# Kernel optimization log

Measured on AMD Instinct MI355X. Metric: run time of the kernel, lower is better.

The kernel has to match this reference:

```python
import jax, jax.numpy as jnp
import numpy as np

TOP_K = 8          # n_activated_experts
ROUTE_SCALE = 2.5  # route_scale


def setup_inputs() -> dict:
    key = jax.random.key(0)
    k1, k2, k3 = jax.random.split(key, 3)
    T, D, E = 16384, 7168, 256
    x = jax.random.normal(k1, (T, D), dtype=jnp.float32)
    # nn.Linear weight layout: [out_features, in_features]
    W = jax.random.normal(k2, (E, D), dtype=jnp.float32) * (1.0 / np.sqrt(D))
    bias = jax.random.normal(k3, (E,), dtype=jnp.float32) * 0.01
    return {"x": x, "W": W, "bias": bias}


def reference(x, W, bias):
    # logits: [T, E] = x [T, D] @ W.T [D, E]
    logits = jnp.einsum("td,ed->te", x, W)
    scores = jax.nn.sigmoid(logits)              # original_scores
    biased = scores + bias                       # bias only affects expert selection
    _, indices = jax.lax.top_k(biased, TOP_K)    # [T, K] int32
    weights = jnp.take_along_axis(scores, indices, axis=-1)  # gather unbiased scores
    weights = weights / jnp.sum(weights, axis=-1, keepdims=True)  # sigmoid renorm
    weights = weights * ROUTE_SCALE
    return weights.astype(x.dtype), indices
```

## Files before the change

### kernel.cpp

```cpp
#include <hip/hip_runtime.h>
#include <cmath>

namespace {

typedef _Float16 half8 __attribute__((ext_vector_type(8)));
typedef float f32x4 __attribute__((ext_vector_type(4)));

constexpr int kTokens = 16384;
constexpr int kD      = 7168;
constexpr int kE      = 256;
constexpr int kTopK   = 8;
constexpr float kRouteScale = 2.5f;

constexpr int BM     = 32;
constexpr int BK     = 32;
constexpr int KSTEP  = 128;
constexpr int NT     = kD / BK;
constexpr int NSTEP  = kD / KSTEP;
constexpr float kS  = 4096.0f;
constexpr float kC  = 0.000244140625f;
constexpr size_t kWsTileB = 32768;
constexpr size_t kWsNeed  = (size_t)NT * kWsTileB;

__device__ inline void convoy_barrier() {
    asm volatile("s_waitcnt lgkmcnt(0)" ::: "memory");
    __builtin_amdgcn_s_barrier();
    asm volatile("" ::: "memory");
}

__global__ void wconv_kernel(const float* __restrict__ W, unsigned char* __restrict__ ws)
{
    const int e = blockIdx.x;
    const int t = threadIdx.x;
    const float* src = W + (size_t)e * kD + (size_t)t * 8;
    float v[8];
    *reinterpret_cast<float4*>(v)     = *reinterpret_cast<const float4*>(src);
    *reinterpret_cast<float4*>(v + 4) = *reinterpret_cast<const float4*>(src + 4);
    half8 h, l;
#pragma unroll
    for (int j = 0; j < 8; ++j) {
        _Float16 hh = (_Float16)v[j];
        h[j] = hh;
        l[j] = (_Float16)((v[j] - (float)hh) * kS);
    }
    const int kt = t >> 2;
    const int kg = t & 3;
    const size_t off = (size_t)kt * kWsTileB +
                       (size_t)(((e >> 4) << 6) + (kg << 4) + (e & 15)) * 16;
    *reinterpret_cast<half8*>(ws + off)         = h;
    *reinterpret_cast<half8*>(ws + off + 16384) = l;
}

__global__ __launch_bounds__(512, 4)
void gate_mfma(const float* __restrict__ x,
               const unsigned char* __restrict__ wst,
               const float* __restrict__ bias,
               float* __restrict__ out)
{
    __shared__ unsigned char lds[32896];

    const int t    = threadIdx.x;
    const int lane = t & 63;
    const int wid  = t >> 6;
    const int kk0  = wid & 3;
    const int m0   = blockIdx.x * BM;
    const int l15  = lane & 15;
    const int lg   = lane >> 4;

    const int srow = t >> 4;
    const int skc  = t & 15;
    const unsigned waddr = (unsigned)(((skc >> 2) << 12) + ((srow >> 4) << 10) +
                                      ((skc & 3) << 8) + ((((srow & 15) ^ skc) & 15) << 4));
    const float* xsrc = x + (size_t)(m0 + srow) * kD + (size_t)(skc * 8);

    const unsigned char* wb = wst + (size_t)(wid * 2) * 1024 + (size_t)lane * 16;

    f32x4 acc0[2][2], acc1[2][2], accL[2][2];
#pragma unroll
    for (int i = 0; i < 2; ++i)
#pragma unroll
        for (int j = 0; j < 2; ++j) {
            acc0[i][j] = f32x4{0.f,0.f,0.f,0.f};
            acc1[i][j] = f32x4{0.f,0.f,0.f,0.f};
            accL[i][j] = f32x4{0.f,0.f,0.f,0.f};
        }

    half8 bh[2][2];
    half8 bl[2][2];
    half8 axh[2][2];
    half8 axm[2][2];

    auto LOADB = [&](int pp, int kt) {
        const unsigned char* p = wb + (size_t)kt * kWsTileB;
        bh[pp][0] = *reinterpret_cast<const half8*>(p);
        bh[pp][1] = *reinterpret_cast<const half8*>(p + 1024);
        bl[pp][0] = *reinterpret_cast<const half8*>(p + 16384);
        bl[pp][1] = *reinterpret_cast<const half8*>(p + 16384 + 1024);
    };
    auto LDA = [&](int pp, unsigned bufc, int kk) {
        const unsigned base = bufc + (unsigned)(kk << 12) + (unsigned)(lg << 8) +
                              (unsigned)((((l15 ^ ((kk << 2) + lg)) & 15) << 4));
        axh[pp][0] = *reinterpret_cast<const half8*>(&lds[base]);
        axh[pp][1] = *reinterpret_cast<const half8*>(&lds[base + 1024]);
        axm[pp][0] = *reinterpret_cast<const half8*>(&lds[base + 2048]);
        axm[pp][1] = *reinterpret_cast<const half8*>(&lds[base + 3072]);
    };
    auto WRITESTEP = [&](unsigned base, const float4& a, const float4& b) {
        float v[8];
        *reinterpret_cast<float4*>(v)     = a;
        *reinterpret_cast<float4*>(v + 4) = b;
        half8 h0, h1;
#pragma unroll
        for (int j = 0; j < 8; ++j) {
            const _Float16 hh = (_Float16)v[j];
            h0[j] = hh;
            h1[j] = (_Float16)((v[j] - (float)hh) * kS);
        }
        *reinterpret_cast<half8*>(&lds[base + waddr])        = h0;
        *reinterpret_cast<half8*>(&lds[base + waddr + 2048]) = h1;
    };

    {
        float4 a = *reinterpret_cast<const float4*>(xsrc);
        float4 b = *reinterpret_cast<const float4*>(xsrc + 4);
        LOADB(0, kk0);
        WRITESTEP(0, a, b);
    }
    convoy_barrier();

    for (int s = 0; s < NSTEP; ++s) {
        const unsigned bufc = (unsigned)((s & 1) << 14);
        const unsigned bufn = (unsigned)(((s + 1) & 1) << 14);
        const bool pre = (s + 1 < NSTEP);

        LDA(0, bufc, kk0);
        float4 nv0{0,0,0,0}, nv1{0,0,0,0};
        if (pre) {
            const float* p = xsrc + (s + 1) * KSTEP;
            nv0 = *reinterpret_cast<const float4*>(p);
            nv1 = *reinterpret_cast<const float4*>(p + 4);
        }

#pragma unroll
        for (int n = 0; n < 4; ++n) {
            const int kk = (kk0 + n) & 3;
            const int pp = n & 1;
            const int kt_next = (n < 3) ? (s * 4 + ((kk0 + n + 1) & 3))
                                        : ((s + 1) * 4 + kk0);
            if (kt_next < NT) LOADB(pp ^ 1, kt_next);
            if (n < 3)        LDA(pp ^ 1, bufc, (kk0 + n + 1) & 3);
#pragma unroll
            for (int i = 0; i < 2; ++i)
#pragma unroll
                for (int j = 0; j < 2; ++j)
                    acc0[i][j] = __builtin_amdgcn_mfma_f32_16x16x32_f16(axh[pp][i], bh[pp][j], acc0[i][j], 0, 0, 0);
#pragma unroll
            for (int i = 0; i < 2; ++i)
#pragma unroll
                for (int j = 0; j < 2; ++j)
                    acc1[i][j] = __builtin_amdgcn_mfma_f32_16x16x32_f16(axm[pp][i], bh[pp][j], acc1[i][j], 0, 0, 0);
#pragma unroll
            for (int i = 0; i < 2; ++i)
#pragma unroll
                for (int j = 0; j < 2; ++j)
                    acc1[i][j] = __builtin_amdgcn_mfma_f32_16x16x32_f16(axh[pp][i], bl[pp][j], acc1[i][j], 0, 0, 0);
        }

        if (pre) WRITESTEP(bufn, nv0, nv1);

        if (((s + 1) & 7) == 0) {
#pragma unroll
            for (int i = 0; i < 2; ++i)
#pragma unroll
                for (int j = 0; j < 2; ++j) {
                    accL[i][j] += acc0[i][j];
                    acc0[i][j] = f32x4{0.f,0.f,0.f,0.f};
                }
        }
        convoy_barrier();
    }

    float (*sc)[257] = reinterpret_cast<float (*)[257]>(lds);
#pragma unroll
    for (int j = 0; j < 2; ++j) {
        const int col  = wid * 32 + j * 16 + l15;
        const float bv = bias[col];
#pragma unroll
        for (int i = 0; i < 2; ++i) {
            f32x4 z = (accL[i][j] + acc0[i][j]) + kC * acc1[i][j];
#pragma unroll
            for (int r = 0; r < 4; ++r) {
                const int row = i * 16 + lg * 4 + r;
                const float s = 1.0f / (1.0f + expf(-z[r]));
                sc[row][col] = s + bv;
            }
        }
    }
    __syncthreads();

    const int rr = t >> 4;
    const int g  = t & 15;

    float cval[kTopK];
    int   cidx[kTopK];

#pragma unroll
    for (int r = 0; r < kTopK; ++r) {
        float best = -INFINITY;
        int   bi   = kE;
        const float* rowp = sc[rr] + g * 16;
#pragma unroll 8
        for (int c = 0; c < 16; ++c) {
            const float v  = rowp[c];
            const int   ci = g * 16 + c;
            if (v > best || (v == best && ci < bi)) { best = v; bi = ci; }
        }
#pragma unroll
        for (int off = 8; off > 0; off >>= 1) {
            const float ov = __shfl_xor(best, off, 16);
            const int   oi = __shfl_xor(bi,   off, 16);
            if (ov > best || (ov == best && oi < bi)) { best = ov; bi = oi; }
        }
        cval[r] = best;
        cidx[r] = bi;
        if ((bi >> 4) == g) sc[rr][bi] = -INFINITY;
    }

    if (g == 0) {
        float uw[kTopK];
        float wsum = 0.0f;
#pragma unroll
        for (int r = 0; r < kTopK; ++r) {
            uw[r] = cval[r] - bias[cidx[r]];
            wsum += uw[r];
        }
        const float scale = kRouteScale / wsum;
        const size_t grow = (size_t)(m0 + rr);
#pragma unroll
        for (int r = 0; r < kTopK; ++r)
            out[grow * kTopK + r] = uw[r] * scale;
#pragma unroll
        for (int r = 0; r < kTopK; ++r)
            out[(size_t)kTokens * kTopK + grow * kTopK + r] = (float)cidx[r];
    }
}

constexpr int FBM = 32;
constexpr int FBK = 32;
constexpr int XS_STRIDE = 36;
constexpr int SC_STRIDE = 260;

__global__ __launch_bounds__(256, 2)
void gate_fused(const float* __restrict__ x,
                const float* __restrict__ W,
                const float* __restrict__ bias,
                float* __restrict__ out)
{
    __shared__ float smem[FBK * XS_STRIDE + FBK * kE];
    float (*xs)[XS_STRIDE] = reinterpret_cast<float (*)[XS_STRIDE]>(smem);
    float (*ws)[kE]        = reinterpret_cast<float (*)[kE]>(smem + FBK * XS_STRIDE);
    float (*sc)[SC_STRIDE] = reinterpret_cast<float (*)[SC_STRIDE]>(smem);

    const int t  = threadIdx.x;
    const int tx = t & 31;
    const int ty = t >> 5;
    const int m0 = blockIdx.x * FBM;
    const int lm = t >> 3;
    const int lc = t & 7;

    float acc[4][8];
    float cmp[4][8];
#pragma unroll
    for (int i = 0; i < 4; ++i)
#pragma unroll
        for (int j = 0; j < 8; ++j) { acc[i][j] = 0.0f; cmp[i][j] = 0.0f; }

    const float* xrow = x + (size_t)(m0 + lm) * kD;
    const float* wrow = W + (size_t)t * kD;

    for (int k0 = 0; k0 < kD; k0 += FBK) {
        float4 xv = *reinterpret_cast<const float4*>(xrow + k0 + 4 * lc);
        float4 wv[8];
#pragma unroll
        for (int i = 0; i < 8; ++i)
            wv[i] = *reinterpret_cast<const float4*>(wrow + k0 + 4 * i);
        __syncthreads();
        xs[4 * lc + 0][lm] = xv.x; xs[4 * lc + 1][lm] = xv.y;
        xs[4 * lc + 2][lm] = xv.z; xs[4 * lc + 3][lm] = xv.w;
#pragma unroll
        for (int i = 0; i < 8; ++i) {
            ws[4 * i + 0][t] = wv[i].x; ws[4 * i + 1][t] = wv[i].y;
            ws[4 * i + 2][t] = wv[i].z; ws[4 * i + 3][t] = wv[i].w;
        }
        __syncthreads();
        float p[4][8];
#pragma unroll
        for (int i = 0; i < 4; ++i)
#pragma unroll
            for (int j = 0; j < 8; ++j) p[i][j] = 0.0f;
#pragma unroll
        for (int k = 0; k < FBK; ++k) {
            float a[4], b[8];
            *reinterpret_cast<float4*>(a)     = *reinterpret_cast<const float4*>(&xs[k][4 * ty]);
            *reinterpret_cast<float4*>(b)     = *reinterpret_cast<const float4*>(&ws[k][4 * tx]);
            *reinterpret_cast<float4*>(b + 4) = *reinterpret_cast<const float4*>(&ws[k][128 + 4 * tx]);
#pragma unroll
            for (int i = 0; i < 4; ++i)
#pragma unroll
                for (int j = 0; j < 8; ++j)
                    p[i][j] = fmaf(a[i], b[j], p[i][j]);
        }
#pragma unroll
        for (int i = 0; i < 4; ++i)
#pragma unroll
            for (int j = 0; j < 8; ++j) {
                const float y = p[i][j] - cmp[i][j];
                const float s = acc[i][j] + y;
                cmp[i][j] = (s - acc[i][j]) - y;
                acc[i][j] = s;
            }
    }
    __syncthreads();
#pragma unroll
    for (int i = 0; i < 4; ++i) {
        const int row = 4 * ty + i;
#pragma unroll
        for (int j = 0; j < 8; ++j) {
            const int col = (j < 4) ? (4 * tx + j) : (128 + 4 * tx + (j - 4));
            const float s = 1.0f / (1.0f + expf(-acc[i][j]));
            sc[row][col] = s + bias[col];
        }
    }
    __syncthreads();
    const int rr = t >> 3;
    const int g  = t & 7;
    float cval[kTopK];
    int   cidx[kTopK];
#pragma unroll
    for (int r = 0; r < kTopK; ++r) {
        float best = -INFINITY;
        int   bi   = kE;
        const float* rowp = sc[rr] + g * 32;
#pragma unroll 8
        for (int c = 0; c < 32; ++c) {
            const float v  = rowp[c];
            const int   ci = g * 32 + c;
            if (v > best || (v == best && ci < bi)) { best = v; bi = ci; }
        }
#pragma unroll
        for (int off = 4; off > 0; off >>= 1) {
            const float ov = __shfl_xor(best, off, 8);
            const int   oi = __shfl_xor(bi,   off, 8);
            if (ov > best || (ov == best && oi < bi)) { best = ov; bi = oi; }
        }
        cval[r] = best; cidx[r] = bi;
        if ((bi >> 5) == g) sc[rr][bi] = -INFINITY;
        __syncthreads();
    }
    if (g == 0) {
        float uw[kTopK];
        float wsum = 0.0f;
#pragma unroll
        for (int r = 0; r < kTopK; ++r) { uw[r] = cval[r] - bias[cidx[r]]; wsum += uw[r]; }
        const float scale = kRouteScale / wsum;
        const size_t grow = (size_t)(m0 + rr);
#pragma unroll
        for (int r = 0; r < kTopK; ++r) out[grow * kTopK + r] = uw[r] * scale;
#pragma unroll
        for (int r = 0; r < kTopK; ++r)
            out[(size_t)kTokens * kTopK + grow * kTopK + r] = (float)cidx[r];
    }
}

}

extern "C" void kernel_launch(void* const* d_in, const int* in_sizes, int n_in,
                              void* d_out, int out_size, void* d_ws, size_t ws_size,
                              hipStream_t stream)
{
    const float* x    = (const float*)d_in[0];
    const float* W    = (const float*)d_in[1];
    const float* bias = (const float*)d_in[2];
    float* out = (float*)d_out;

    if (ws_size >= kWsNeed) {
        unsigned char* ws = (unsigned char*)d_ws;
        hipLaunchKernelGGL(wconv_kernel, dim3(kE), dim3(kD / 8), 0, stream, W, ws);
        hipLaunchKernelGGL(gate_mfma, dim3(kTokens / BM), dim3(512), 0, stream, x, ws, bias, out);
    } else {
        hipLaunchKernelGGL(gate_fused, dim3(kTokens / FBM), dim3(256), 0, stream, x, W, bias, out);
    }
}
```

Before: 278.6 us.

## Double per-block token tile to 64 rows and halve the K step

```diff
diff --git a/kernel.cpp b/kernel.cpp
--- a/kernel.cpp
+++ b/kernel.cpp
@@ -12,9 +12,9 @@
 constexpr int kTopK   = 8;
 constexpr float kRouteScale = 2.5f;
 
-constexpr int BM     = 32;
+constexpr int BM     = 64;
 constexpr int BK     = 32;
-constexpr int KSTEP  = 128;
+constexpr int KSTEP  = 64;
 constexpr int NT     = kD / BK;
 constexpr int NSTEP  = kD / KSTEP;
 constexpr float kS  = 4096.0f;
@@ -51,33 +51,32 @@
     *reinterpret_cast<half8*>(ws + off + 16384) = l;
 }
 
-__global__ __launch_bounds__(512, 4)
+__global__ __launch_bounds__(512, 2)
 void gate_mfma(const float* __restrict__ x,
                const unsigned char* __restrict__ wst,
                const float* __restrict__ bias,
                float* __restrict__ out)
 {
-    __shared__ unsigned char lds[32896];
+    __shared__ unsigned char lds[65792];
 
     const int t    = threadIdx.x;
     const int lane = t & 63;
     const int wid  = t >> 6;
-    const int kk0  = wid & 3;
     const int m0   = blockIdx.x * BM;
     const int l15  = lane & 15;
     const int lg   = lane >> 4;
 
-    const int srow = t >> 4;
-    const int skc  = t & 15;
-    const unsigned waddr = (unsigned)(((skc >> 2) << 12) + ((srow >> 4) << 10) +
-                                      ((skc & 3) << 8) + ((((srow & 15) ^ skc) & 15) << 4));
+    const int srow = t >> 3;
+    const int skc  = t & 7;
+    const unsigned waddr = (unsigned)(((skc >> 2) << 13) + ((srow >> 4) << 10) +
+                                      ((skc & 3) << 8) + (((srow & 15) ^ skc) << 4));
     const float* xsrc = x + (size_t)(m0 + srow) * kD + (size_t)(skc * 8);
 
     const unsigned char* wb = wst + (size_t)(wid * 2) * 1024 + (size_t)lane * 16;
 
-    f32x4 acc0[2][2], acc1[2][2], accL[2][2];
-#pragma unroll
-    for (int i = 0; i < 2; ++i)
+    f32x4 acc0[4][2], acc1[4][2], accL[4][2];
+#pragma unroll
+    for (int i = 0; i < 4; ++i)
 #pragma unroll
         for (int j = 0; j < 2; ++j) {
             acc0[i][j] = f32x4{0.f,0.f,0.f,0.f};
@@ -87,8 +86,8 @@
 
     half8 bh[2][2];
     half8 bl[2][2];
-    half8 axh[2][2];
-    half8 axm[2][2];
+    half8 axh[2][4];
+    half8 axm[2][4];
 
     auto LOADB = [&](int pp, int kt) {
         const unsigned char* p = wb + (size_t)kt * kWsTileB;
@@ -98,12 +97,13 @@
         bl[pp][1] = *reinterpret_cast<const half8*>(p + 16384 + 1024);
     };
     auto LDA = [&](int pp, unsigned bufc, int kk) {
-        const unsigned base = bufc + (unsigned)(kk << 12) + (unsigned)(lg << 8) +
+        const unsigned base = bufc + (unsigned)(kk << 13) + (unsigned)(lg << 8) +
                               (unsigned)((((l15 ^ ((kk << 2) + lg)) & 15) << 4));
-        axh[pp][0] = *reinterpret_cast<const half8*>(&lds[base]);
-        axh[pp][1] = *reinterpret_cast<const half8*>(&lds[base + 1024]);
-        axm[pp][0] = *reinterpret_cast<const half8*>(&lds[base + 2048]);
-        axm[pp][1] = *reinterpret_cast<const half8*>(&lds[base + 3072]);
+#pragma unroll
+        for (int i = 0; i < 4; ++i) {
+            axh[pp][i] = *reinterpret_cast<const half8*>(&lds[base + i * 1024]);
+            axm[pp][i] = *reinterpret_cast<const half8*>(&lds[base + i * 1024 + 4096]);
+        }
     };
     auto WRITESTEP = [&](unsigned base, const float4& a, const float4& b) {
         float v[8];
@@ -117,13 +117,13 @@
             h1[j] = (_Float16)((v[j] - (float)hh) * kS);
         }
         *reinterpret_cast<half8*>(&lds[base + waddr])        = h0;
-        *reinterpret_cast<half8*>(&lds[base + waddr + 2048]) = h1;
+        *reinterpret_cast<half8*>(&lds[base + waddr + 4096]) = h1;
     };
 
     {
         float4 a = *reinterpret_cast<const float4*>(xsrc);
         float4 b = *reinterpret_cast<const float4*>(xsrc + 4);
-        LOADB(0, kk0);
+        LOADB(0, 0);
         WRITESTEP(0, a, b);
     }
     convoy_barrier();
@@ -133,7 +133,7 @@
         const unsigned bufn = (unsigned)(((s + 1) & 1) << 14);
         const bool pre = (s + 1 < NSTEP);
 
-        LDA(0, bufc, kk0);
+        LDA(0, bufc, 0);
         float4 nv0{0,0,0,0}, nv1{0,0,0,0};
         if (pre) {
             const float* p = xsrc + (s + 1) * KSTEP;
@@ -142,35 +142,32 @@
         }
 
 #pragma unroll
-        for (int n = 0; n < 4; ++n) {
-            const int kk = (kk0 + n) & 3;
-            const int pp = n & 1;
-            const int kt_next = (n < 3) ? (s * 4 + ((kk0 + n + 1) & 3))
-                                        : ((s + 1) * 4 + kk0);
-            if (kt_next < NT) LOADB(pp ^ 1, kt_next);
-            if (n < 3)        LDA(pp ^ 1, bufc, (kk0 + n + 1) & 3);
-#pragma unroll
-            for (int i = 0; i < 2; ++i)
+        for (int kk = 0; kk < 2; ++kk) {
+            const int kt_next = s * 2 + kk + 1;
+            if (kt_next < NT) LOADB(kk ^ 1, kt_next);
+            if (kk == 0)      LDA(1, bufc, 1);
+#pragma unroll
+            for (int i = 0; i < 4; ++i)
 #pragma unroll
                 for (int j = 0; j < 2; ++j)
-                    acc0[i][j] = __builtin_amdgcn_mfma_f32_16x16x32_f16(axh[pp][i], bh[pp][j], acc0[i][j], 0, 0, 0);
-#pragma unroll
-            for (int i = 0; i < 2; ++i)
+                    acc0[i][j] = __builtin_amdgcn_mfma_f32_16x16x32_f16(axh[kk][i], bh[kk][j], acc0[i][j], 0, 0, 0);
+#pragma unroll
+            for (int i = 0; i < 4; ++i)
 #pragma unroll
                 for (int j = 0; j < 2; ++j)
-                    acc1[i][j] = __builtin_amdgcn_mfma_f32_16x16x32_f16(axm[pp][i], bh[pp][j], acc1[i][j], 0, 0, 0);
-#pragma unroll
-            for (int i = 0; i < 2; ++i)
+                    acc1[i][j] = __builtin_amdgcn_mfma_f32_16x16x32_f16(axm[kk][i], bh[kk][j], acc1[i][j], 0, 0, 0);
+#pragma unroll
+            for (int i = 0; i < 4; ++i)
 #pragma unroll
                 for (int j = 0; j < 2; ++j)
-                    acc1[i][j] = __builtin_amdgcn_mfma_f32_16x16x32_f16(axh[pp][i], bl[pp][j], acc1[i][j], 0, 0, 0);
+                    acc1[i][j] = __builtin_amdgcn_mfma_f32_16x16x32_f16(axh[kk][i], bl[kk][j], acc1[i][j], 0, 0, 0);
         }
 
         if (pre) WRITESTEP(bufn, nv0, nv1);
 
-        if (((s + 1) & 7) == 0) {
-#pragma unroll
-            for (int i = 0; i < 2; ++i)
+        if (((s + 1) & 15) == 0) {
+#pragma unroll
+            for (int i = 0; i < 4; ++i)
 #pragma unroll
                 for (int j = 0; j < 2; ++j) {
                     accL[i][j] += acc0[i][j];
@@ -186,7 +183,7 @@
         const int col  = wid * 32 + j * 16 + l15;
         const float bv = bias[col];
 #pragma unroll
-        for (int i = 0; i < 2; ++i) {
+        for (int i = 0; i < 4; ++i) {
             f32x4 z = (accL[i][j] + acc0[i][j]) + kC * acc1[i][j];
 #pragma unroll
             for (int r = 0; r < 4; ++r) {
@@ -198,8 +195,8 @@
     }
     __syncthreads();
 
-    const int rr = t >> 4;
-    const int g  = t & 15;
+    const int rr = t >> 3;
+    const int g  = t & 7;
 
     float cval[kTopK];
     int   cidx[kTopK];
@@ -208,22 +205,22 @@
     for (int r = 0; r < kTopK; ++r) {
         float best = -INFINITY;
         int   bi   = kE;
-        const float* rowp = sc[rr] + g * 16;
+        const float* rowp = sc[rr] + g * 32;
 #pragma unroll 8
-        for (int c = 0; c < 16; ++c) {
+        for (int c = 0; c < 32; ++c) {
             const float v  = rowp[c];
-            const int   ci = g * 16 + c;
+            const int   ci = g * 32 + c;
             if (v > best || (v == best && ci < bi)) { best = v; bi = ci; }
         }
 #pragma unroll
-        for (int off = 8; off > 0; off >>= 1) {
-            const float ov = __shfl_xor(best, off, 16);
-            const int   oi = __shfl_xor(bi,   off, 16);
+        for (int off = 4; off > 0; off >>= 1) {
+            const float ov = __shfl_xor(best, off, 8);
+            const int   oi = __shfl_xor(bi,   off, 8);
             if (ov > best || (ov == best && oi < bi)) { best = ov; bi = oi; }
         }
         cval[r] = best;
         cidx[r] = bi;
-        if ((bi >> 4) == g) sc[rr][bi] = -INFINITY;
+        if ((bi >> 5) == g) sc[rr][bi] = -INFINITY;
     }
 
     if (g == 0) {
```

Measured after the change: 242.9 us. 12.8% less time.

## Double token tile to 64 rows with 16 waves sharing each W fragment

Applied to the files above, without the earlier changes.

```diff
diff --git a/kernel.cpp b/kernel.cpp
--- a/kernel.cpp
+++ b/kernel.cpp
@@ -12,9 +12,9 @@
 constexpr int kTopK   = 8;
 constexpr float kRouteScale = 2.5f;
 
-constexpr int BM     = 32;
+constexpr int BM     = 64;
 constexpr int BK     = 32;
-constexpr int KSTEP  = 128;
+constexpr int KSTEP  = 64;
 constexpr int NT     = kD / BK;
 constexpr int NSTEP  = kD / KSTEP;
 constexpr float kS  = 4096.0f;
@@ -51,29 +51,31 @@
     *reinterpret_cast<half8*>(ws + off + 16384) = l;
 }
 
-__global__ __launch_bounds__(512, 4)
+__global__ __launch_bounds__(1024, 4)
 void gate_mfma(const float* __restrict__ x,
                const unsigned char* __restrict__ wst,
                const float* __restrict__ bias,
                float* __restrict__ out)
 {
-    __shared__ unsigned char lds[32896];
+    __shared__ unsigned char lds[65792];
 
     const int t    = threadIdx.x;
     const int lane = t & 63;
-    const int wid  = t >> 6;
-    const int kk0  = wid & 3;
+    const int w    = t >> 6;
+    const int cg   = w & 7;
+    const int rg   = w >> 3;
     const int m0   = blockIdx.x * BM;
     const int l15  = lane & 15;
     const int lg   = lane >> 4;
 
-    const int srow = t >> 4;
-    const int skc  = t & 15;
-    const unsigned waddr = (unsigned)(((skc >> 2) << 12) + ((srow >> 4) << 10) +
-                                      ((skc & 3) << 8) + ((((srow & 15) ^ skc) & 15) << 4));
+    const int srow = (t >> 3) & 63;
+    const int skc  = t & 7;
+    const unsigned waddr = (unsigned)(((skc >> 2) << 13) + ((srow >> 4) << 10) +
+                                      ((skc & 3) << 8) + (((srow & 15) ^ skc) << 4));
     const float* xsrc = x + (size_t)(m0 + srow) * kD + (size_t)(skc * 8);
-
-    const unsigned char* wb = wst + (size_t)(wid * 2) * 1024 + (size_t)lane * 16;
+    const bool stager = (t < 512);
+
+    const unsigned char* wb = wst + (size_t)(cg * 2) * 1024 + (size_t)lane * 16;
 
     f32x4 acc0[2][2], acc1[2][2], accL[2][2];
 #pragma unroll
@@ -98,12 +100,13 @@
         bl[pp][1] = *reinterpret_cast<const half8*>(p + 16384 + 1024);
     };
     auto LDA = [&](int pp, unsigned bufc, int kk) {
-        const unsigned base = bufc + (unsigned)(kk << 12) + (unsigned)(lg << 8) +
+        const unsigned base = bufc + (unsigned)(kk << 13) + (unsigned)((rg * 2) << 10) +
+                              (unsigned)(lg << 8) +
                               (unsigned)((((l15 ^ ((kk << 2) + lg)) & 15) << 4));
         axh[pp][0] = *reinterpret_cast<const half8*>(&lds[base]);
         axh[pp][1] = *reinterpret_cast<const half8*>(&lds[base + 1024]);
-        axm[pp][0] = *reinterpret_cast<const half8*>(&lds[base + 2048]);
-        axm[pp][1] = *reinterpret_cast<const half8*>(&lds[base + 3072]);
+        axm[pp][0] = *reinterpret_cast<const half8*>(&lds[base + 4096]);
+        axm[pp][1] = *reinterpret_cast<const half8*>(&lds[base + 4096 + 1024]);
     };
     auto WRITESTEP = [&](unsigned base, const float4& a, const float4& b) {
         float v[8];
@@ -117,14 +120,16 @@
             h1[j] = (_Float16)((v[j] - (float)hh) * kS);
         }
         *reinterpret_cast<half8*>(&lds[base + waddr])        = h0;
-        *reinterpret_cast<half8*>(&lds[base + waddr + 2048]) = h1;
+        *reinterpret_cast<half8*>(&lds[base + waddr + 4096]) = h1;
     };
 
     {
-        float4 a = *reinterpret_cast<const float4*>(xsrc);
-        float4 b = *reinterpret_cast<const float4*>(xsrc + 4);
-        LOADB(0, kk0);
-        WRITESTEP(0, a, b);
+        LOADB(0, 0);
+        if (stager) {
+            float4 a = *reinterpret_cast<const float4*>(xsrc);
+            float4 b = *reinterpret_cast<const float4*>(xsrc + 4);
+            WRITESTEP(0, a, b);
+        }
     }
     convoy_barrier();
 
@@ -133,42 +138,39 @@
         const unsigned bufn = (unsigned)(((s + 1) & 1) << 14);
         const bool pre = (s + 1 < NSTEP);
 
-        LDA(0, bufc, kk0);
+        LDA(0, bufc, 0);
         float4 nv0{0,0,0,0}, nv1{0,0,0,0};
-        if (pre) {
+        if (pre && stager) {
             const float* p = xsrc + (s + 1) * KSTEP;
             nv0 = *reinterpret_cast<const float4*>(p);
             nv1 = *reinterpret_cast<const float4*>(p + 4);
         }
 
 #pragma unroll
-        for (int n = 0; n < 4; ++n) {
-            const int kk = (kk0 + n) & 3;
-            const int pp = n & 1;
-            const int kt_next = (n < 3) ? (s * 4 + ((kk0 + n + 1) & 3))
-                                        : ((s + 1) * 4 + kk0);
-            if (kt_next < NT) LOADB(pp ^ 1, kt_next);
-            if (n < 3)        LDA(pp ^ 1, bufc, (kk0 + n + 1) & 3);
+        for (int kk = 0; kk < 2; ++kk) {
+            const int kt_next = s * 2 + kk + 1;
+            if (kt_next < NT) LOADB(kk ^ 1, kt_next);
+            if (kk == 0)      LDA(1, bufc, 1);
 #pragma unroll
             for (int i = 0; i < 2; ++i)
 #pragma unroll
                 for (int j = 0; j < 2; ++j)
-                    acc0[i][j] = __builtin_amdgcn_mfma_f32_16x16x32_f16(axh[pp][i], bh[pp][j], acc0[i][j], 0, 0, 0);
+                    acc0[i][j] = __builtin_amdgcn_mfma_f32_16x16x32_f16(axh[kk][i], bh[kk][j], acc0[i][j], 0, 0, 0);
 #pragma unroll
             for (int i = 0; i < 2; ++i)
 #pragma unroll
                 for (int j = 0; j < 2; ++j)
-                    acc1[i][j] = __builtin_amdgcn_mfma_f32_16x16x32_f16(axm[pp][i], bh[pp][j], acc1[i][j], 0, 0, 0);
+                    acc1[i][j] = __builtin_amdgcn_mfma_f32_16x16x32_f16(axm[kk][i], bh[kk][j], acc1[i][j], 0, 0, 0);
 #pragma unroll
             for (int i = 0; i < 2; ++i)
 #pragma unroll
                 for (int j = 0; j < 2; ++j)
-                    acc1[i][j] = __builtin_amdgcn_mfma_f32_16x16x32_f16(axh[pp][i], bl[pp][j], acc1[i][j], 0, 0, 0);
-        }
-
-        if (pre) WRITESTEP(bufn, nv0, nv1);
-
-        if (((s + 1) & 7) == 0) {
+                    acc1[i][j] = __builtin_amdgcn_mfma_f32_16x16x32_f16(axh[kk][i], bl[kk][j], acc1[i][j], 0, 0, 0);
+        }
+
+        if (pre && stager) WRITESTEP(bufn, nv0, nv1);
+
+        if (((s + 1) & 15) == 0) {
 #pragma unroll
             for (int i = 0; i < 2; ++i)
 #pragma unroll
@@ -183,14 +185,14 @@
     float (*sc)[257] = reinterpret_cast<float (*)[257]>(lds);
 #pragma unroll
     for (int j = 0; j < 2; ++j) {
-        const int col  = wid * 32 + j * 16 + l15;
+        const int col  = cg * 32 + j * 16 + l15;
         const float bv = bias[col];
 #pragma unroll
         for (int i = 0; i < 2; ++i) {
             f32x4 z = (accL[i][j] + acc0[i][j]) + kC * acc1[i][j];
 #pragma unroll
             for (int r = 0; r < 4; ++r) {
-                const int row = i * 16 + lg * 4 + r;
+                const int row = rg * 32 + i * 16 + lg * 4 + r;
                 const float s = 1.0f / (1.0f + expf(-z[r]));
                 sc[row][col] = s + bv;
             }
@@ -386,7 +388,7 @@
     if (ws_size >= kWsNeed) {
         unsigned char* ws = (unsigned char*)d_ws;
         hipLaunchKernelGGL(wconv_kernel, dim3(kE), dim3(kD / 8), 0, stream, W, ws);
-        hipLaunchKernelGGL(gate_mfma, dim3(kTokens / BM), dim3(512), 0, stream, x, ws, bias, out);
+        hipLaunchKernelGGL(gate_mfma, dim3(kTokens / BM), dim3(1024), 0, stream, x, ws, bias, out);
     } else {
         hipLaunchKernelGGL(gate_fused, dim3(kTokens / FBM), dim3(256), 0, stream, x, W, bias, out);
     }
```

Measured after the change: 250.3 us. 10.2% less time.
